# Kernel tuning notes

Measured on AMD Instinct MI355X. Metric: run time of the kernel, lower is better.

Reference implementation:

```python
import jax, jax.numpy as jnp
import numpy as np

B, T = 8, 512
ACT, EMB, DET, HID, NST = 32, 1024, 1024, 1024, 16
STO, CLS = 32, 32
UNIMIX = 0.01


def _ln(x, g, b):
    m = x.mean(-1, keepdims=True)
    v = x.var(-1, keepdims=True)
    return (x - m) / jnp.sqrt(v + 1e-5) * g + b


def _lnsilu(x, g, b):
    return jax.nn.silu(_ln(x, g, b))


def setup_inputs() -> dict:
    key = jax.random.key(0)
    ks = iter(jax.random.split(key, 40))

    def lin(din, dout):
        return jax.random.normal(next(ks), (din, dout), jnp.float32) / np.sqrt(din)

    actions = jax.random.normal(next(ks), (B, T, ACT), jnp.float32)
    embeds = jax.random.normal(next(ks), (B, T, EMB), jnp.float32)
    # pre_ssm: Linear(ACT,HID) + LayerNormSiLU(HID)
    W_pre, b_pre = lin(ACT, HID), jnp.zeros(HID)
    g_pre, bb_pre = jnp.ones(HID), jnp.zeros(HID)
    W_emb = lin(EMB, HID)  # bias=False
    W_in, b_in = lin(HID, 2 * DET), jnp.zeros(2 * DET)
    W_dt = lin(DET, DET)
    # dt bias init: inverse-softplus of dt ~ LogUniform(1e-3, 0.1)
    u = jax.random.uniform(next(ks), (DET,), jnp.float32)
    dt_init = jnp.exp(u * (np.log(0.1) - np.log(1e-3)) + np.log(1e-3))
    b_dt = dt_init + jnp.log(-jnp.expm1(-dt_init))
    W_B, W_C = lin(DET, NST), lin(DET, NST)
    A_log = jnp.broadcast_to(
        jnp.log(jnp.arange(1, NST + 1, dtype=jnp.float32)), (DET, NST)
    ) + jnp.zeros((DET, NST))
    Dp = jnp.ones(DET)
    g_out, b_out = jnp.ones(DET), jnp.zeros(DET)
    # prior_net: Linear(DET,HID)+LNSiLU+Linear(HID,STO*CLS)
    W_pr1, b_pr1 = lin(DET, HID), jnp.zeros(HID)
    g_pr, bb_pr = jnp.ones(HID), jnp.zeros(HID)
    W_pr2, b_pr2 = lin(HID, STO * CLS), jnp.zeros(STO * CLS)
    # post_net: Linear(DET+EMB,HID)+LNSiLU+Linear(HID,STO*CLS)
    W_po1, b_po1 = lin(DET + EMB, HID), jnp.zeros(HID)
    g_po, bb_po = jnp.ones(HID), jnp.zeros(HID)
    W_po2, b_po2 = lin(HID, STO * CLS), jnp.zeros(STO * CLS)
    return dict(actions=actions, embeds=embeds, W_pre=W_pre, b_pre=b_pre,
                g_pre=g_pre, bb_pre=bb_pre, W_emb=W_emb, W_in=W_in, b_in=b_in,
                W_dt=W_dt, b_dt=b_dt, W_B=W_B, W_C=W_C, A_log=A_log, Dp=Dp,
                g_out=g_out, b_out=b_out, W_pr1=W_pr1, b_pr1=b_pr1, g_pr=g_pr,
                bb_pr=bb_pr, W_pr2=W_pr2, b_pr2=b_pr2, W_po1=W_po1, b_po1=b_po1,
                g_po=g_po, bb_po=bb_po, W_po2=W_po2, b_po2=b_po2)


def reference(actions, embeds, W_pre, b_pre, g_pre, bb_pre, W_emb, W_in, b_in,
              W_dt, b_dt, W_B, W_C, A_log, Dp, g_out, b_out, W_pr1, b_pr1,
              g_pr, bb_pr, W_pr2, b_pr2, W_po1, b_po1, g_po, bb_po, W_po2, b_po2):
    # input projections
    x = _lnsilu(actions @ W_pre + b_pre, g_pre, bb_pre) + embeds @ W_emb  # (B,T,HID)
    x = x.transpose(1, 0, 2)  # (T,B,HID)
    xz = x @ W_in + b_in
    x_ssm, x_gate = xz[..., :DET], xz[..., DET:]
    dt = jax.nn.softplus(x_ssm @ W_dt + b_dt)        # (T,B,DET)
    Bp = x_ssm @ W_B                                  # (T,B,NST)
    Cp = x_ssm @ W_C                                  # (T,B,NST)
    A = -jnp.exp(A_log)                               # (DET,NST)
    gates = jnp.exp(dt[..., None] * A)                # (T,B,DET,NST)
    values = (dt * x_ssm)[..., None] * Bp[:, :, None, :]

    # linear recurrence h[t] = g[t]*h[t-1] + v[t] via associative scan
    def comb(a, c):
        g1, v1 = a
        g2, v2 = c
        return (g1 * g2, g2 * v1 + v2)

    _, h = jax.lax.associative_scan(comb, (gates, values), axis=0)
    y = jnp.einsum('tbdn,tbn->tbd', h, Cp) + Dp * x_ssm
    y = y * jax.nn.silu(x_gate)
    deter = _ln(y, g_out, b_out)                      # (T,B,DET)

    # prior / post heads
    prior = _lnsilu(deter @ W_pr1 + b_pr1, g_pr, bb_pr) @ W_pr2 + b_pr2
    emb_t = embeds.transpose(1, 0, 2)
    post_in = jnp.concatenate([deter, emb_t], -1)
    post = _lnsilu(post_in @ W_po1 + b_po1, g_po, bb_po) @ W_po2 + b_po2
    # unimix transform of post logits (deterministic part of _categorical)
    p = jax.nn.softmax(post.reshape(T, B, STO, CLS), -1)
    p = (1.0 - UNIMIX) * p + UNIMIX / CLS
    post_u = jnp.log(p + 1e-8).reshape(T, B, STO * CLS)
    return jnp.concatenate([deter, prior, post_u], -1)  # (T,B,DET+2*STO*CLS)
```

## Files before the change

### kernel.cpp

```cpp
#include <hip/hip_runtime.h>
#include <hip/hip_bf16.h>
#include <math.h>


typedef __bf16 bf16_t;
typedef __bf16 bf16x8 __attribute__((ext_vector_type(8)));
typedef float f32x4 __attribute__((ext_vector_type(4)));

#define B_   8
#define T_   512
#define R_   4096
#define HID_ 1024
#define NC_  32
#define CL_  16

static __device__ __forceinline__ float bf2f(bf16_t x) { return (float)x; }
static __device__ __forceinline__ bf16_t f2bf(float x) { return (bf16_t)x; }
static __device__ __forceinline__ float ldany(const void* p, size_t i, bool isb) {
  return isb ? bf2f(((const bf16_t*)p)[i]) : ((const float*)p)[i];
}

typedef __attribute__((address_space(3))) unsigned int lds_u32;
typedef const __attribute__((address_space(1))) unsigned int glb_u32;
static __device__ __forceinline__ void gld16(const bf16_t* g, bf16_t* l) {
  __builtin_amdgcn_global_load_lds((glb_u32*)g, (lds_u32*)l, 16, 0, 0);
}

__global__ void detect_k(const unsigned int* __restrict__ dp_raw, int* __restrict__ flag) {
  if (threadIdx.x == 0) *flag = (dp_raw[0] == 0x3F803F80u) ? 1 : 0;
}

struct CvtArgs {
  const void* src[17];
  float* dst[17];
  int n[17];
};
__global__ __launch_bounds__(256) void cvt_vecs(CvtArgs a, const int* __restrict__ flag) {
  const bool isb = (*flag != 0);
  int v = blockIdx.y;
  const void* s = a.src[v];
  float* d = a.dst[v];
  int n = a.n[v];
  for (int i = blockIdx.x * 256 + threadIdx.x; i < n; i += 8 * 256)
    d[i] = ldany(s, i, isb);
}

__device__ __forceinline__ void block_sum2(float& s, float& ss) {
#pragma unroll
  for (int off = 32; off > 0; off >>= 1) {
    s  += __shfl_down(s, off, 64);
    ss += __shfl_down(ss, off, 64);
  }
  __shared__ float red[8];
  int tid = threadIdx.x;
  int wave = tid >> 6, lane = tid & 63;
  if (lane == 0) { red[wave] = s; red[4 + wave] = ss; }
  __syncthreads();
  s  = red[0] + red[1] + red[2] + red[3];
  ss = red[4] + red[5] + red[6] + red[7];
}

struct TrArgs {
  const void* src[8];
  bf16_t* dst[8];
  int K[8], N[8];
  int tile0[9];
};
__global__ void tr_batch(TrArgs a, const int* __restrict__ flag) {
  __shared__ float tile[32][33];
  const bool isb = (*flag != 0);
  int bid = blockIdx.x;
  int m = 0;
#pragma unroll
  for (int q = 0; q < 7; ++q) if (bid >= a.tile0[q + 1]) m = q + 1;
  int local = bid - a.tile0[m];
  int K = a.K[m], N = a.N[m];
  int ntx = N >> 5;
  int n0 = (local % ntx) * 32, k0 = (local / ntx) * 32;
  const void* src = a.src[m];
  bf16_t* dst = a.dst[m];
  int tx = threadIdx.x, ty = threadIdx.y;
#pragma unroll
  for (int i = 0; i < 4; ++i) {
    size_t idx = (size_t)(k0 + ty + i * 8) * N + n0 + tx;
    tile[ty + i * 8][tx] = ldany(src, idx, isb);
  }
  __syncthreads();
#pragma unroll
  for (int i = 0; i < 4; ++i)
    dst[(size_t)(n0 + ty + i * 8) * K + k0 + tx] = f2bf(tile[tx][ty + i * 8]);
}

__global__ __launch_bounds__(256) void bc_build(const void* __restrict__ W_B,
                                                const void* __restrict__ W_C,
                                                bf16_t* __restrict__ WTdtbc,
                                                const int* __restrict__ flag) {
  const bool isb = (*flag != 0);
  int idx = blockIdx.x * 256 + threadIdx.x;
  int r = idx >> 10, k = idx & 1023;
  float v = 0.f;
  if (r < 16)      v = ldany(W_B, k * 16 + r, isb);
  else if (r < 32) v = ldany(W_C, k * 16 + (r - 16), isb);
  WTdtbc[(size_t)(1024 + r) * 1024 + k] = f2bf(v);
}

__global__ __launch_bounds__(256) void reorder_emb(const void* __restrict__ emb,
                                                   bf16_t* __restrict__ embT,
                                                   const int* __restrict__ flag) {
  const bool isb = (*flag != 0);
  int r = blockIdx.x, tid = threadIdx.x;
  int t = r >> 3, b = r & 7;
  size_t base = (size_t)(b * T_ + t) * 1024;
#pragma unroll
  for (int i = 0; i < 4; ++i) {
    int c = i * 256 + tid;
    embT[(size_t)r * 1024 + c] = f2bf(ldany(emb, base + c, isb));
  }
}

__global__ __launch_bounds__(256) void reorder_act(const void* __restrict__ act,
                                                   bf16_t* __restrict__ actA,
                                                   const int* __restrict__ flag) {
  const bool isb = (*flag != 0);
  int i = blockIdx.x * 256 + threadIdx.x;
  int r = i >> 5, k = i & 31;
  int t = r >> 3, b = r & 7;
  actA[(size_t)r * 32 + k] = f2bf(ldany(act, (size_t)(b * T_ + t) * 32 + k, isb));
}

enum { EPI_ADD_BF16 = 0, EPI_XZ = 1, EPI_BIAS_F32 = 3, EPI_PRIOR = 4, EPI_DTBC = 6 };

struct GemmArgs {
  const bf16_t* A;
  const bf16_t* Bt;
  int K;
  int N;
  int bnN;
  const float* bias;
  const bf16_t* addh;
  float* outf0;
  float* outf1;
  float* outf2;
  bf16_t* outh0;
  bf16_t* outh1;
  void* outv;
  const int* flag;
};

template <int EPI>
__global__ __launch_bounds__(256) void gemm_t(GemmArgs g) {
  __shared__ __align__(16) bf16_t As[64 * 32];
  __shared__ __align__(16) bf16_t Bs[64 * 32];
  const int tid = threadIdx.x;
  const int wave = tid >> 6, lane = tid & 63;
  const int K = g.K;

  const int per = gridDim.x >> 3;
  const int idx = (blockIdx.x & 7) * per + (blockIdx.x >> 3);
  const int bm = idx / g.bnN, bn = idx % g.bnN;

  f32x4 acc[2][2] = {};

  const int srow = tid >> 2;
  const int sblk = (tid & 3) ^ ((srow >> 1) & 3);
  const bf16_t* Ap = g.A  + (size_t)(bm * 64 + srow) * K + sblk * 8;
  const bf16_t* Bp = g.Bt + (size_t)(bn * 64 + srow) * K + sblk * 8;
  bf16_t* AsW = &As[tid * 8];
  bf16_t* BsW = &Bs[tid * 8];

  const int wm = (wave >> 1) * 32, wn = (wave & 1) * 32;
  const int fm = lane & 15;
  const int swz = (lane >> 4) ^ ((fm >> 1) & 3);

  for (int k0 = 0; k0 < K; k0 += 32) {
    gld16(Ap + k0, AsW);
    gld16(Bp + k0, BsW);
    __syncthreads();
    bf16x8 af[2], bfr[2];
#pragma unroll
    for (int i = 0; i < 2; ++i)
      af[i] = *(const bf16x8*)&As[((wm + i * 16 + fm) * 4 + swz) * 8];
#pragma unroll
    for (int j = 0; j < 2; ++j)
      bfr[j] = *(const bf16x8*)&Bs[((wn + j * 16 + fm) * 4 + swz) * 8];
#pragma unroll
    for (int i = 0; i < 2; ++i)
#pragma unroll
      for (int j = 0; j < 2; ++j)
        acc[i][j] = __builtin_amdgcn_mfma_f32_16x16x32_bf16(af[i], bfr[j], acc[i][j], 0, 0, 0);
    __syncthreads();
  }

  const bool out_bf = (EPI == EPI_PRIOR) ? (*g.flag != 0) : false;
  const int em = (lane >> 4) * 4, en = lane & 15;
#pragma unroll
  for (int i = 0; i < 2; ++i) {
#pragma unroll
    for (int j = 0; j < 2; ++j) {
#pragma unroll
      for (int v = 0; v < 4; ++v) {
        int row = bm * 64 + wm + i * 16 + em + v;
        int col = bn * 64 + wn + j * 16 + en;
        float x = acc[i][j][v];
        if constexpr (EPI == EPI_ADD_BF16) {
          size_t o = (size_t)row * g.N + col;
          g.outh0[o] = f2bf(x + bf2f(g.addh[o]));
        } else if constexpr (EPI == EPI_XZ) {
          float val = x + g.bias[col];
          if (col < 1024) g.outh0[(size_t)row * 1024 + col] = f2bf(val);
          else            g.outh1[(size_t)row * 1024 + (col - 1024)] = f2bf(val);
        } else if constexpr (EPI == EPI_BIAS_F32) {
          g.outf0[(size_t)row * g.N + col] = x + g.bias[col];
        } else if constexpr (EPI == EPI_DTBC) {
          if (col < 1024) {
            float val = x + g.bias[col];
            float sp = (val > 20.f) ? val : log1pf(__expf(val));
            g.outf0[(size_t)row * 1024 + col] = sp;
          } else if (col < 1040) {
            g.outf1[(size_t)row * 16 + (col - 1024)] = x;
          } else if (col < 1056) {
            g.outf2[(size_t)row * 16 + (col - 1040)] = x;
          }
        } else {
          float val = x + g.bias[col];
          size_t o = (size_t)row * 3072 + 1024 + col;
          if (out_bf) ((bf16_t*)g.outv)[o] = f2bf(val);
          else        ((float*)g.outv)[o]  = val;
        }
      }
    }
  }
}

__global__ __launch_bounds__(256) void scan_p1(const float* __restrict__ dt,
                                               const bf16_t* __restrict__ xsh,
                                               const float* __restrict__ Bp,
                                               const float* __restrict__ A_log,
                                               float* __restrict__ Gp,
                                               float* __restrict__ Hl) {
  int idx = blockIdx.x * 256 + threadIdx.x;
  int d = idx & 1023;
  int cb = idx >> 10;
  int b = cb & 7, c = cb >> 3;
  float Ad[16];
#pragma unroll
  for (int n = 0; n < 16; ++n) Ad[n] = -__expf(A_log[d * 16 + n]);
  float h[16] = {};
  float dts = 0.f;
  int r0 = c * CL_ * 8 + b;
  for (int tl = 0; tl < CL_; ++tl) {
    int r = r0 + tl * 8;
    size_t off = (size_t)r * 1024 + d;
    float dtv = dt[off], xv = bf2f(xsh[off]);
    float dtx = dtv * xv;
    dts += dtv;
    const float4* Bp4 = (const float4*)(Bp + r * 16);
    float4 b4[4] = {Bp4[0], Bp4[1], Bp4[2], Bp4[3]};
    const float* bv = (const float*)b4;
#pragma unroll
    for (int n = 0; n < 16; ++n) {
      float gg = __expf(dtv * Ad[n]);
      h[n] = gg * h[n] + dtx * bv[n];
    }
  }
  float* gp = Gp + (size_t)idx * 16;
  float* hl = Hl + (size_t)idx * 16;
#pragma unroll
  for (int q = 0; q < 4; ++q) {
    float4 gq, hq;
    gq.x = __expf(dts * Ad[q * 4 + 0]); gq.y = __expf(dts * Ad[q * 4 + 1]);
    gq.z = __expf(dts * Ad[q * 4 + 2]); gq.w = __expf(dts * Ad[q * 4 + 3]);
    hq.x = h[q * 4 + 0]; hq.y = h[q * 4 + 1]; hq.z = h[q * 4 + 2]; hq.w = h[q * 4 + 3];
    ((float4*)gp)[q] = gq;
    ((float4*)hl)[q] = hq;
  }
}

__global__ __launch_bounds__(256) void scan_p2(float* __restrict__ GpCin,
                                               const float* __restrict__ Hl) {
  int j = blockIdx.x * 256 + threadIdx.x;
  float carry = 0.f;
#pragma unroll
  for (int c = 0; c < NC_; ++c) {
    size_t o = (size_t)c * 131072 + j;
    float gv = GpCin[o], hl = Hl[o];
    GpCin[o] = carry;
    carry = gv * carry + hl;
  }
}

__global__ __launch_bounds__(256) void scan_p3(const float* __restrict__ dt,
                                               const bf16_t* __restrict__ xsh,
                                               const bf16_t* __restrict__ xg,
                                               const float* __restrict__ Bp,
                                               const float* __restrict__ Cp,
                                               const float* __restrict__ A_log,
                                               const float* __restrict__ Dp,
                                               const float* __restrict__ Cin,
                                               float* __restrict__ y) {
  int idx = blockIdx.x * 256 + threadIdx.x;
  int d = idx & 1023;
  int cb = idx >> 10;
  int b = cb & 7, c = cb >> 3;
  float Ad[16];
#pragma unroll
  for (int n = 0; n < 16; ++n) Ad[n] = -__expf(A_log[d * 16 + n]);
  float Dd = Dp[d];
  float h[16];
  const float4* Ci4 = (const float4*)(Cin + (size_t)idx * 16);
#pragma unroll
  for (int q = 0; q < 4; ++q) {
    float4 cq = Ci4[q];
    h[q * 4 + 0] = cq.x; h[q * 4 + 1] = cq.y; h[q * 4 + 2] = cq.z; h[q * 4 + 3] = cq.w;
  }
  int r0 = c * CL_ * 8 + b;
  for (int tl = 0; tl < CL_; ++tl) {
    int r = r0 + tl * 8;
    size_t off = (size_t)r * 1024 + d;
    float dtv = dt[off], xv = bf2f(xsh[off]), gv = bf2f(xg[off]);
    float dtx = dtv * xv;
    const float4* Bp4 = (const float4*)(Bp + r * 16);
    const float4* Cp4 = (const float4*)(Cp + r * 16);
    float4 b4[4] = {Bp4[0], Bp4[1], Bp4[2], Bp4[3]};
    float4 c4[4] = {Cp4[0], Cp4[1], Cp4[2], Cp4[3]};
    const float* bv = (const float*)b4;
    const float* cv = (const float*)c4;
    float yv = 0.f;
#pragma unroll
    for (int n = 0; n < 16; ++n) {
      float gg = __expf(dtv * Ad[n]);
      h[n] = gg * h[n] + dtx * bv[n];
      yv += h[n] * cv[n];
    }
    yv += Dd * xv;
    float sg = gv / (1.f + __expf(-gv));
    y[off] = yv * sg;
  }
}

template <int MODE>
__global__ __launch_bounds__(256) void ln_k(const float* __restrict__ in,
                                            const float* __restrict__ gw,
                                            const float* __restrict__ bw,
                                            bf16_t* __restrict__ out0,
                                            void* __restrict__ out1,
                                            const bf16_t* __restrict__ embT,
                                            bf16_t* __restrict__ post_in,
                                            const int* __restrict__ flag) {
  const bool out_bf = (MODE == 0) ? (*flag != 0) : false;
  int r = blockIdx.x, tid = threadIdx.x;
  float v[4];
  float s = 0.f, ss = 0.f;
#pragma unroll
  for (int i = 0; i < 4; ++i) {
    v[i] = in[(size_t)r * 1024 + i * 256 + tid];
    s += v[i]; ss += v[i] * v[i];
  }
  block_sum2(s, ss);
  float mean = s * (1.f / 1024.f);
  float var  = ss * (1.f / 1024.f) - mean * mean;
  float rstd = rsqrtf(var + 1e-5f);
#pragma unroll
  for (int i = 0; i < 4; ++i) {
    int c = i * 256 + tid;
    float yv = (v[i] - mean) * rstd * gw[c] + bw[c];
    if constexpr (MODE == 1) yv = yv / (1.f + __expf(-yv));
    out0[(size_t)r * 1024 + c] = f2bf(yv);
    if constexpr (MODE == 0) {
      size_t o = (size_t)r * 3072 + c;
      if (out_bf) ((bf16_t*)out1)[o] = f2bf(yv);
      else        ((float*)out1)[o]  = yv;
      post_in[(size_t)r * 2048 + c] = f2bf(yv);
      post_in[(size_t)r * 2048 + 1024 + c] = embT[(size_t)r * 1024 + c];
    }
  }
}

__global__ __launch_bounds__(256) void softmax_k(const float* __restrict__ logits,
                                                 void* __restrict__ out,
                                                 const int* __restrict__ flag) {
  const bool out_bf = (*flag != 0);
  int idx = blockIdx.x * 256 + threadIdx.x;
  int r = idx >> 5, grp = idx & 31;
  const float* p = logits + (size_t)r * 1024 + grp * 32;
  float x[32];
  float m = -1e30f;
#pragma unroll
  for (int j = 0; j < 32; ++j) { x[j] = p[j]; m = fmaxf(m, x[j]); }
  float sum = 0.f;
#pragma unroll
  for (int j = 0; j < 32; ++j) { x[j] = __expf(x[j] - m); sum += x[j]; }
  float inv = 0.99f / sum;
  size_t base = (size_t)r * 3072 + 2048 + grp * 32;
#pragma unroll
  for (int j = 0; j < 32; ++j) {
    float val = logf(x[j] * inv + (0.01f / 32.f) + 1e-8f);
    if (out_bf) ((bf16_t*)out)[base + j] = f2bf(val);
    else        ((float*)out)[base + j]  = val;
  }
}

extern "C" void kernel_launch(void* const* d_in, const int* in_sizes, int n_in,
                              void* d_out, int out_size, void* d_ws, size_t ws_size,
                              hipStream_t stream) {
  (void)in_sizes; (void)n_in; (void)out_size; (void)ws_size;
  const void* actions = d_in[0];
  const void* embeds  = d_in[1];
  const void* W_pre   = d_in[2];
  const void* b_pre   = d_in[3];
  const void* g_pre   = d_in[4];
  const void* bb_pre  = d_in[5];
  const void* W_emb   = d_in[6];
  const void* W_in    = d_in[7];
  const void* b_in    = d_in[8];
  const void* W_dt    = d_in[9];
  const void* b_dt    = d_in[10];
  const void* W_B     = d_in[11];
  const void* W_C     = d_in[12];
  const void* A_log   = d_in[13];
  const void* Dp      = d_in[14];
  const void* g_out   = d_in[15];
  const void* b_out   = d_in[16];
  const void* W_pr1   = d_in[17];
  const void* b_pr1   = d_in[18];
  const void* g_pr    = d_in[19];
  const void* bb_pr   = d_in[20];
  const void* W_pr2   = d_in[21];
  const void* b_pr2   = d_in[22];
  const void* W_po1   = d_in[23];
  const void* b_po1   = d_in[24];
  const void* g_po    = d_in[25];
  const void* bb_po   = d_in[26];
  const void* W_po2   = d_in[27];
  const void* b_po2   = d_in[28];

  char* ws = (char*)d_ws;
  const size_t KB = 1024;
  bf16_t* WTemb  = (bf16_t*)(ws + 0 * KB);
  bf16_t* WTin   = (bf16_t*)(ws + 2048 * KB);
  bf16_t* WTdtbc = (bf16_t*)(ws + 6144 * KB);
  bf16_t* WTpr1  = (bf16_t*)(ws + 8320 * KB);
  bf16_t* WTpr2  = (bf16_t*)(ws + 10368 * KB);
  bf16_t* WTpo1  = (bf16_t*)(ws + 12416 * KB);
  bf16_t* WTpo2  = (bf16_t*)(ws + 16512 * KB);
  bf16_t* embT   = (bf16_t*)(ws + 18560 * KB);
  float*  F1     = (float*)(ws + 26752 * KB);
  float*  F2     = (float*)(ws + 43136 * KB);
  float*  F5     = (float*)(ws + 59520 * KB);
  bf16_t* B8     = (bf16_t*)(ws + 75904 * KB);
  bf16_t* B9     = (bf16_t*)(ws + 84096 * KB);
  bf16_t* G8     = (bf16_t*)(ws + 92288 * KB);
  float*  BpB    = (float*)(ws + 100480 * KB);
  float*  CpB    = (float*)(ws + 100736 * KB);
  float*  Hl     = (float*)(ws + 59520 * KB);
  float*  Gp     = (float*)(ws + 43136 * KB);
  char* cb = ws + 100992 * KB;
  int*   flag    = (int*)(cb);                cb += 256;
  float* Alog_f  = (float*)(cb);              cb += 16384 * 4;
  float* Dp_f    = (float*)(cb);              cb += 1024 * 4;
  float* bpre_f  = (float*)(cb);              cb += 1024 * 4;
  float* gpre_f  = (float*)(cb);              cb += 1024 * 4;
  float* bbpre_f = (float*)(cb);              cb += 1024 * 4;
  float* bin_f   = (float*)(cb);              cb += 2048 * 4;
  float* bdt_f   = (float*)(cb);              cb += 1024 * 4;
  float* gout_f  = (float*)(cb);              cb += 1024 * 4;
  float* bout_f  = (float*)(cb);              cb += 1024 * 4;
  float* bpr1_f  = (float*)(cb);              cb += 1024 * 4;
  float* gpr_f   = (float*)(cb);              cb += 1024 * 4;
  float* bbpr_f  = (float*)(cb);              cb += 1024 * 4;
  float* bpr2_f  = (float*)(cb);              cb += 1024 * 4;
  float* bpo1_f  = (float*)(cb);              cb += 1024 * 4;
  float* gpo_f   = (float*)(cb);              cb += 1024 * 4;
  float* bbpo_f  = (float*)(cb);              cb += 1024 * 4;
  float* bpo2_f  = (float*)(cb);              cb += 1024 * 4;
  bf16_t* actA   = (bf16_t*)(cb);             cb += 4096 * 32 * 2;
  bf16_t* WTpre  = (bf16_t*)(cb);             cb += 1024 * 32 * 2;

  detect_k<<<1, 64, 0, stream>>>((const unsigned int*)Dp, flag);

  CvtArgs ca{};
  const void* srcs[17] = {A_log, Dp, b_pre, g_pre, bb_pre, b_in, b_dt,
                          g_out, b_out, b_pr1, g_pr, bb_pr, b_pr2,
                          b_po1, g_po, bb_po, b_po2};
  float* dsts[17] = {Alog_f, Dp_f, bpre_f, gpre_f, bbpre_f, bin_f, bdt_f,
                     gout_f, bout_f, bpr1_f, gpr_f, bbpr_f, bpr2_f,
                     bpo1_f, gpo_f, bbpo_f, bpo2_f};
  int ns[17] = {16384, 1024, 1024, 1024, 1024, 2048, 1024,
                1024, 1024, 1024, 1024, 1024, 1024,
                1024, 1024, 1024, 1024};
  for (int i = 0; i < 17; ++i) { ca.src[i] = srcs[i]; ca.dst[i] = dsts[i]; ca.n[i] = ns[i]; }
  cvt_vecs<<<dim3(8, 17), 256, 0, stream>>>(ca, flag);

  {
    TrArgs ta{};
    const void* tsrc[8] = {W_emb, W_in, W_dt, W_pr1, W_pr2, W_po1, W_po2, W_pre};
    bf16_t* tdst[8] = {WTemb, WTin, WTdtbc, WTpr1, WTpr2, WTpo1, WTpo2, WTpre};
    int tK[8] = {1024, 1024, 1024, 1024, 1024, 2048, 1024, 32};
    int tN[8] = {1024, 2048, 1024, 1024, 1024, 1024, 1024, 1024};
    int off = 0;
    for (int i = 0; i < 8; ++i) {
      ta.src[i] = tsrc[i]; ta.dst[i] = tdst[i]; ta.K[i] = tK[i]; ta.N[i] = tN[i];
      ta.tile0[i] = off; off += (tK[i] >> 5) * (tN[i] >> 5);
    }
    ta.tile0[8] = off;
    tr_batch<<<off, dim3(32, 8), 0, stream>>>(ta, flag);
  }
  bc_build<<<256, 256, 0, stream>>>(W_B, W_C, WTdtbc, flag);

  reorder_emb<<<R_, 256, 0, stream>>>(embeds, embT, flag);
  reorder_act<<<512, 256, 0, stream>>>(actions, actA, flag);

  {
    GemmArgs a{}; a.A = actA; a.Bt = WTpre; a.K = 32; a.N = 1024; a.bnN = 16;
    a.bias = bpre_f; a.outf0 = F5;
    gemm_t<EPI_BIAS_F32><<<1024, 256, 0, stream>>>(a);
  }
  ln_k<1><<<R_, 256, 0, stream>>>(F5, gpre_f, bbpre_f, B8, nullptr,
                                  nullptr, nullptr, flag);
  {
    GemmArgs a{}; a.A = embT; a.Bt = WTemb; a.K = 1024; a.N = 1024; a.bnN = 16;
    a.addh = B8; a.outh0 = G8;
    gemm_t<EPI_ADD_BF16><<<1024, 256, 0, stream>>>(a);
  }
  {
    GemmArgs a{}; a.A = G8; a.Bt = WTin; a.K = 1024; a.N = 2048; a.bnN = 32;
    a.bias = bin_f; a.outh0 = B9; a.outh1 = B8;
    gemm_t<EPI_XZ><<<2048, 256, 0, stream>>>(a);
  }
  {
    GemmArgs a{}; a.A = B9; a.Bt = WTdtbc; a.K = 1024; a.N = 1088; a.bnN = 17;
    a.bias = bdt_f; a.outf0 = F1; a.outf1 = BpB; a.outf2 = CpB;
    gemm_t<EPI_DTBC><<<1088, 256, 0, stream>>>(a);
  }
  scan_p1<<<1024, 256, 0, stream>>>(F1, B9, BpB, Alog_f, Gp, Hl);
  scan_p2<<<512, 256, 0, stream>>>(Gp, Hl);
  scan_p3<<<1024, 256, 0, stream>>>(F1, B9, B8, BpB, CpB, Alog_f, Dp_f, Gp, F5);
  ln_k<0><<<R_, 256, 0, stream>>>(F5, gout_f, bout_f, B9, d_out,
                                  embT, (bf16_t*)F5, flag);
  {
    GemmArgs a{}; a.A = B9; a.Bt = WTpr1; a.K = 1024; a.N = 1024; a.bnN = 16;
    a.bias = bpr1_f; a.outf0 = F1;
    gemm_t<EPI_BIAS_F32><<<1024, 256, 0, stream>>>(a);
  }
  ln_k<1><<<R_, 256, 0, stream>>>(F1, gpr_f, bbpr_f, B8, nullptr,
                                  nullptr, nullptr, flag);
  {
    GemmArgs a{}; a.A = B8; a.Bt = WTpr2; a.K = 1024; a.N = 1024; a.bnN = 16;
    a.bias = bpr2_f; a.outv = d_out; a.flag = flag;
    gemm_t<EPI_PRIOR><<<1024, 256, 0, stream>>>(a);
  }
  {
    GemmArgs a{}; a.A = (bf16_t*)F5; a.Bt = WTpo1; a.K = 2048; a.N = 1024; a.bnN = 16;
    a.bias = bpo1_f; a.outf0 = F2;
    gemm_t<EPI_BIAS_F32><<<1024, 256, 0, stream>>>(a);
  }
  ln_k<1><<<R_, 256, 0, stream>>>(F2, gpo_f, bbpo_f, B8, nullptr,
                                  nullptr, nullptr, flag);
  {
    GemmArgs a{}; a.A = B8; a.Bt = WTpo2; a.K = 1024; a.N = 1024; a.bnN = 16;
    a.bias = bpo2_f; a.outf0 = F1;
    gemm_t<EPI_BIAS_F32><<<1024, 256, 0, stream>>>(a);
  }
  softmax_k<<<512, 256, 0, stream>>>(F1, d_out, flag);
}
```

Baseline: 490.3 us.

## Group prior/post head GEMMs, fuse LN pairs and softmax into GEMM epilogue

Merges the three small prep kernels into one launch. The prior and post first-layer GEMMs now run in one grouped kernel, their two LayerNorm-SiLU passes run in one kernel, and the second-layer GEMMs are grouped with the unimix softmax/log folded into the post GEMM epilogue using lane shuffles. This cuts kernel launches and serial dependencies, drops an fp32 logits round trip, and lets independent GEMMs fill more CUs. The risk is uneven block cost in the grouped kernels, since the post GEMM has K=2048 versus 1024 for the prior.

```diff
diff --git a/kernel.cpp b/kernel.cpp
--- a/kernel.cpp
+++ b/kernel.cpp
@@ -91,44 +91,42 @@
     dst[(size_t)(n0 + ty + i * 8) * K + k0 + tx] = f2bf(tile[tx][ty + i * 8]);
 }
 
-__global__ __launch_bounds__(256) void bc_build(const void* __restrict__ W_B,
-                                                const void* __restrict__ W_C,
-                                                bf16_t* __restrict__ WTdtbc,
-                                                const int* __restrict__ flag) {
+__global__ __launch_bounds__(256) void prep_misc(const void* __restrict__ emb,
+                                                 bf16_t* __restrict__ embT,
+                                                 const void* __restrict__ act,
+                                                 bf16_t* __restrict__ actA,
+                                                 const void* __restrict__ W_B,
+                                                 const void* __restrict__ W_C,
+                                                 bf16_t* __restrict__ WTdtbc,
+                                                 const int* __restrict__ flag) {
   const bool isb = (*flag != 0);
-  int idx = blockIdx.x * 256 + threadIdx.x;
-  int r = idx >> 10, k = idx & 1023;
-  float v = 0.f;
-  if (r < 16)      v = ldany(W_B, k * 16 + r, isb);
-  else if (r < 32) v = ldany(W_C, k * 16 + (r - 16), isb);
-  WTdtbc[(size_t)(1024 + r) * 1024 + k] = f2bf(v);
-}
-
-__global__ __launch_bounds__(256) void reorder_emb(const void* __restrict__ emb,
-                                                   bf16_t* __restrict__ embT,
-                                                   const int* __restrict__ flag) {
-  const bool isb = (*flag != 0);
-  int r = blockIdx.x, tid = threadIdx.x;
-  int t = r >> 3, b = r & 7;
-  size_t base = (size_t)(b * T_ + t) * 1024;
-#pragma unroll
-  for (int i = 0; i < 4; ++i) {
-    int c = i * 256 + tid;
-    embT[(size_t)r * 1024 + c] = f2bf(ldany(emb, base + c, isb));
-  }
-}
-
-__global__ __launch_bounds__(256) void reorder_act(const void* __restrict__ act,
-                                                   bf16_t* __restrict__ actA,
-                                                   const int* __restrict__ flag) {
-  const bool isb = (*flag != 0);
-  int i = blockIdx.x * 256 + threadIdx.x;
-  int r = i >> 5, k = i & 31;
-  int t = r >> 3, b = r & 7;
-  actA[(size_t)r * 32 + k] = f2bf(ldany(act, (size_t)(b * T_ + t) * 32 + k, isb));
-}
-
-enum { EPI_ADD_BF16 = 0, EPI_XZ = 1, EPI_BIAS_F32 = 3, EPI_PRIOR = 4, EPI_DTBC = 6 };
+  int bid = blockIdx.x, tid = threadIdx.x;
+  if (bid < 4096) {
+    int r = bid;
+    int t = r >> 3, b = r & 7;
+    size_t base = (size_t)(b * T_ + t) * 1024;
+#pragma unroll
+    for (int i = 0; i < 4; ++i) {
+      int c = i * 256 + tid;
+      embT[(size_t)r * 1024 + c] = f2bf(ldany(emb, base + c, isb));
+    }
+  } else if (bid < 4608) {
+    int i = (bid - 4096) * 256 + tid;
+    int r = i >> 5, k = i & 31;
+    int t = r >> 3, b = r & 7;
+    actA[(size_t)r * 32 + k] = f2bf(ldany(act, (size_t)(b * T_ + t) * 32 + k, isb));
+  } else {
+    int idx = (bid - 4608) * 256 + tid;
+    int r = idx >> 10, k = idx & 1023;
+    float v = 0.f;
+    if (r < 16)      v = ldany(W_B, k * 16 + r, isb);
+    else if (r < 32) v = ldany(W_C, k * 16 + (r - 16), isb);
+    WTdtbc[(size_t)(1024 + r) * 1024 + k] = f2bf(v);
+  }
+}
+
+enum { EPI_ADD_BF16 = 0, EPI_XZ = 1, EPI_BIAS_F32 = 3, EPI_PRIOR = 4,
+       EPI_DTBC = 6, EPI_SMAX = 7 };
 
 struct GemmArgs {
   const bf16_t* A;
@@ -148,15 +146,11 @@
 };
 
 template <int EPI>
-__global__ __launch_bounds__(256) void gemm_t(GemmArgs g) {
-  __shared__ __align__(16) bf16_t As[64 * 32];
-  __shared__ __align__(16) bf16_t Bs[64 * 32];
+__device__ __forceinline__ void gemm_body(const GemmArgs& g, int idx,
+                                          bf16_t* As, bf16_t* Bs) {
   const int tid = threadIdx.x;
   const int wave = tid >> 6, lane = tid & 63;
   const int K = g.K;
-
-  const int per = gridDim.x >> 3;
-  const int idx = (blockIdx.x & 7) * per + (blockIdx.x >> 3);
   const int bm = idx / g.bnN, bn = idx % g.bnN;
 
   f32x4 acc[2][2] = {};
@@ -191,8 +185,38 @@
     __syncthreads();
   }
 
+  const int em = (lane >> 4) * 4, en = lane & 15;
+
+  if constexpr (EPI == EPI_SMAX) {
+    const bool ob = (*g.flag != 0);
+#pragma unroll
+    for (int i = 0; i < 2; ++i) {
+#pragma unroll
+      for (int v = 0; v < 4; ++v) {
+        int row = bm * 64 + wm + i * 16 + em + v;
+        int c0 = bn * 64 + wn + en;
+        int c1 = c0 + 16;
+        float x0 = acc[i][0][v] + g.bias[c0];
+        float x1 = acc[i][1][v] + g.bias[c1];
+        float m = fmaxf(x0, x1);
+#pragma unroll
+        for (int d = 1; d < 16; d <<= 1) m = fmaxf(m, __shfl_xor(m, d, 64));
+        float e0 = __expf(x0 - m), e1 = __expf(x1 - m);
+        float s = e0 + e1;
+#pragma unroll
+        for (int d = 1; d < 16; d <<= 1) s += __shfl_xor(s, d, 64);
+        float inv = 0.99f / s;
+        float p0 = logf(e0 * inv + (0.01f / 32.f) + 1e-8f);
+        float p1 = logf(e1 * inv + (0.01f / 32.f) + 1e-8f);
+        size_t o0 = (size_t)row * 3072 + 2048 + c0;
+        if (ob) { ((bf16_t*)g.outv)[o0] = f2bf(p0); ((bf16_t*)g.outv)[o0 + 16] = f2bf(p1); }
+        else    { ((float*)g.outv)[o0]  = p0;       ((float*)g.outv)[o0 + 16]  = p1; }
+      }
+    }
+    return;
+  }
+
   const bool out_bf = (EPI == EPI_PRIOR) ? (*g.flag != 0) : false;
-  const int em = (lane >> 4) * 4, en = lane & 15;
 #pragma unroll
   for (int i = 0; i < 2; ++i) {
 #pragma unroll
@@ -232,6 +256,26 @@
   }
 }
 
+template <int EPI>
+__global__ __launch_bounds__(256) void gemm_t(GemmArgs g) {
+  __shared__ __align__(16) bf16_t As[64 * 32];
+  __shared__ __align__(16) bf16_t Bs[64 * 32];
+  const int per = gridDim.x >> 3;
+  const int idx = (blockIdx.x & 7) * per + (blockIdx.x >> 3);
+  gemm_body<EPI>(g, idx, As, Bs);
+}
+
+struct GrpArgs { GemmArgs g0, g1; int tiles0; };
+template <int E0, int E1>
+__global__ __launch_bounds__(256) void gemm_g2(GrpArgs ga) {
+  __shared__ __align__(16) bf16_t As[64 * 32];
+  __shared__ __align__(16) bf16_t Bs[64 * 32];
+  const int per = gridDim.x >> 3;
+  const int idx = (blockIdx.x & 7) * per + (blockIdx.x >> 3);
+  if (idx < ga.tiles0) gemm_body<E0>(ga.g0, idx, As, Bs);
+  else                 gemm_body<E1>(ga.g1, idx - ga.tiles0, As, Bs);
+}
+
 __global__ __launch_bounds__(256) void scan_p1(const float* __restrict__ dt,
                                                const bf16_t* __restrict__ xsh,
                                                const float* __restrict__ Bp,
@@ -376,27 +420,35 @@
   }
 }
 
-__global__ __launch_bounds__(256) void softmax_k(const float* __restrict__ logits,
-                                                 void* __restrict__ out,
-                                                 const int* __restrict__ flag) {
-  const bool out_bf = (*flag != 0);
-  int idx = blockIdx.x * 256 + threadIdx.x;
-  int r = idx >> 5, grp = idx & 31;
-  const float* p = logits + (size_t)r * 1024 + grp * 32;
-  float x[32];
-  float m = -1e30f;
-#pragma unroll
-  for (int j = 0; j < 32; ++j) { x[j] = p[j]; m = fmaxf(m, x[j]); }
-  float sum = 0.f;
-#pragma unroll
-  for (int j = 0; j < 32; ++j) { x[j] = __expf(x[j] - m); sum += x[j]; }
-  float inv = 0.99f / sum;
-  size_t base = (size_t)r * 3072 + 2048 + grp * 32;
-#pragma unroll
-  for (int j = 0; j < 32; ++j) {
-    float val = logf(x[j] * inv + (0.01f / 32.f) + 1e-8f);
-    if (out_bf) ((bf16_t*)out)[base + j] = f2bf(val);
-    else        ((float*)out)[base + j]  = val;
+__global__ __launch_bounds__(256) void ln2_k(const float* __restrict__ in0,
+                                             const float* __restrict__ in1,
+                                             const float* __restrict__ g0,
+                                             const float* __restrict__ b0,
+                                             const float* __restrict__ g1,
+                                             const float* __restrict__ b1,
+                                             bf16_t* __restrict__ o0,
+                                             bf16_t* __restrict__ o1) {
+  int r = blockIdx.x, tid = threadIdx.x;
+  const float* in; const float* gw; const float* bw; bf16_t* out; int rr;
+  if (r < 4096) { in = in0; gw = g0; bw = b0; out = o0; rr = r; }
+  else          { in = in1; gw = g1; bw = b1; out = o1; rr = r - 4096; }
+  float v[4];
+  float s = 0.f, ss = 0.f;
+#pragma unroll
+  for (int i = 0; i < 4; ++i) {
+    v[i] = in[(size_t)rr * 1024 + i * 256 + tid];
+    s += v[i]; ss += v[i] * v[i];
+  }
+  block_sum2(s, ss);
+  float mean = s * (1.f / 1024.f);
+  float var  = ss * (1.f / 1024.f) - mean * mean;
+  float rstd = rsqrtf(var + 1e-5f);
+#pragma unroll
+  for (int i = 0; i < 4; ++i) {
+    int c = i * 256 + tid;
+    float yv = (v[i] - mean) * rstd * gw[c] + bw[c];
+    yv = yv / (1.f + __expf(-yv));
+    out[(size_t)rr * 1024 + c] = f2bf(yv);
   }
 }
 
@@ -505,10 +557,8 @@
     ta.tile0[8] = off;
     tr_batch<<<off, dim3(32, 8), 0, stream>>>(ta, flag);
   }
-  bc_build<<<256, 256, 0, stream>>>(W_B, W_C, WTdtbc, flag);
-
-  reorder_emb<<<R_, 256, 0, stream>>>(embeds, embT, flag);
-  reorder_act<<<512, 256, 0, stream>>>(actions, actA, flag);
+  prep_misc<<<4864, 256, 0, stream>>>(embeds, embT, actions, actA,
+                                      W_B, W_C, WTdtbc, flag);
 
   {
     GemmArgs a{}; a.A = actA; a.Bt = WTpre; a.K = 32; a.N = 1024; a.bnN = 16;
@@ -538,28 +588,22 @@
   ln_k<0><<<R_, 256, 0, stream>>>(F5, gout_f, bout_f, B9, d_out,
                                   embT, (bf16_t*)F5, flag);
   {
-    GemmArgs a{}; a.A = B9; a.Bt = WTpr1; a.K = 1024; a.N = 1024; a.bnN = 16;
-    a.bias = bpr1_f; a.outf0 = F1;
-    gemm_t<EPI_BIAS_F32><<<1024, 256, 0, stream>>>(a);
-  }
-  ln_k<1><<<R_, 256, 0, stream>>>(F1, gpr_f, bbpr_f, B8, nullptr,
-                                  nullptr, nullptr, flag);
+    GrpArgs ga{};
+    ga.g0.A = B9;            ga.g0.Bt = WTpr1; ga.g0.K = 1024; ga.g0.N = 1024;
+    ga.g0.bnN = 16;          ga.g0.bias = bpr1_f; ga.g0.outf0 = F1;
+    ga.g1.A = (bf16_t*)F5;   ga.g1.Bt = WTpo1; ga.g1.K = 2048; ga.g1.N = 1024;
+    ga.g1.bnN = 16;          ga.g1.bias = bpo1_f; ga.g1.outf0 = F2;
+    ga.tiles0 = 1024;
+    gemm_g2<EPI_BIAS_F32, EPI_BIAS_F32><<<2048, 256, 0, stream>>>(ga);
+  }
+  ln2_k<<<2 * R_, 256, 0, stream>>>(F1, F2, gpr_f, bbpr_f, gpo_f, bbpo_f, B8, G8);
   {
-    GemmArgs a{}; a.A = B8; a.Bt = WTpr2; a.K = 1024; a.N = 1024; a.bnN = 16;
-    a.bias = bpr2_f; a.outv = d_out; a.flag = flag;
-    gemm_t<EPI_PRIOR><<<1024, 256, 0, stream>>>(a);
-  }
-  {
-    GemmArgs a{}; a.A = (bf16_t*)F5; a.Bt = WTpo1; a.K = 2048; a.N = 1024; a.bnN = 16;
-    a.bias = bpo1_f; a.outf0 = F2;
-    gemm_t<EPI_BIAS_F32><<<1024, 256, 0, stream>>>(a);
-  }
-  ln_k<1><<<R_, 256, 0, stream>>>(F2, gpo_f, bbpo_f, B8, nullptr,
-                                  nullptr, nullptr, flag);
-  {
-    GemmArgs a{}; a.A = B8; a.Bt = WTpo2; a.K = 1024; a.N = 1024; a.bnN = 16;
-    a.bias = bpo2_f; a.outf0 = F1;
-    gemm_t<EPI_BIAS_F32><<<1024, 256, 0, stream>>>(a);
-  }
-  softmax_k<<<512, 256, 0, stream>>>(F1, d_out, flag);
-}
+    GrpArgs ga{};
+    ga.g0.A = B8; ga.g0.Bt = WTpr2; ga.g0.K = 1024; ga.g0.N = 1024;
+    ga.g0.bnN = 16; ga.g0.bias = bpr2_f; ga.g0.outv = d_out; ga.g0.flag = flag;
+    ga.g1.A = G8; ga.g1.Bt = WTpo2; ga.g1.K = 1024; ga.g1.N = 1024;
+    ga.g1.bnN = 16; ga.g1.bias = bpo2_f; ga.g1.outv = d_out; ga.g1.flag = flag;
+    ga.tiles0 = 1024;
+    gemm_g2<EPI_PRIOR, EPI_SMAX><<<2048, 256, 0, stream>>>(ga);
+  }
+}
```

Result: faster. 472.6 us (-3.6%).
